# Performance work log

Hardware: AMD Instinct MI355X
Metric: run time of the kernel (lower is better)

Reference implementation:

```python
import jax, jax.numpy as jnp
import numpy as np

IMPOSSIBLE = -10000.0  # DataConfig.IMPOSSIBLE_SCORE
B, L, V, E, H, T = 64, 512, 50000, 256, 512, 32


def setup_inputs() -> dict:
    key = jax.random.key(0)
    ks = jax.random.split(key, 15)
    s = 0.05
    return {
        "sents": jax.random.randint(ks[0], (B, L), 0, V),
        "lengths": jnp.full((B,), L, dtype=jnp.int32),
        "targets": jax.random.randint(ks[1], (B, L, T), 0, 2).astype(jnp.int32),
        "emb": jax.random.normal(ks[2], (V, E), jnp.float32) * s,
        "Wih_f": jax.random.normal(ks[3], (4 * H, E), jnp.float32) * s,
        "Whh_f": jax.random.normal(ks[4], (4 * H, H), jnp.float32) * s,
        "b_f": jax.random.normal(ks[5], (4 * H,), jnp.float32) * s,
        "Wih_b": jax.random.normal(ks[6], (4 * H, E), jnp.float32) * s,
        "Whh_b": jax.random.normal(ks[7], (4 * H, H), jnp.float32) * s,
        "b_b": jax.random.normal(ks[8], (4 * H,), jnp.float32) * s,
        "W_out": jax.random.normal(ks[9], (T, 2 * H), jnp.float32) * s,
        "b_out": jax.random.normal(ks[10], (T,), jnp.float32) * s,
        "start_trans": jax.random.normal(ks[11], (T,), jnp.float32),
        "end_trans": jax.random.normal(ks[12], (T,), jnp.float32),
        "trans": jnp.ones((T, T), jnp.float32) / T,
    }


def _lstm_dir(xW, Whh, reverse):
    # xW: (L, B, 4H) = x @ Wih.T + b, precomputed (the big GEMM, done once)
    h0 = jnp.zeros((xW.shape[1], Whh.shape[1]), xW.dtype)
    def step(carry, xw):
        h, c = carry
        g = xw + h @ Whh.T
        i, f, gg, o = jnp.split(g, 4, axis=-1)  # torch gate order i,f,g,o
        c = jax.nn.sigmoid(f) * c + jax.nn.sigmoid(i) * jnp.tanh(gg)
        h = jax.nn.sigmoid(o) * jnp.tanh(c)
        return (h, c), h
    _, hs = jax.lax.scan(step, (h0, h0), xW, reverse=reverse)
    return hs  # (L, B, H), in original time order


def _denominator(em, trans, start, end):
    # em: (L, B, T); CRF partition function via forward algorithm (mask = all ones)
    alpha0 = start + em[0]
    def step(alpha, e):
        inner = alpha[:, :, None] + trans[None] + e[:, None, :]  # (B, T, T)
        return jax.nn.logsumexp(inner, axis=1), None
    alpha, _ = jax.lax.scan(step, alpha0, em[1:])
    return jax.nn.logsumexp(alpha + end[None, :], axis=-1)  # (B,)


def _numerator(em, pt, trans, start, end):
    # em: (L, B, T); pt: (L, B, T) binary possible-tag mask (float)
    alpha0 = start + em[0]
    alpha0 = jnp.where(pt[0] == 0, IMPOSSIBLE, alpha0)
    def step(alpha, inputs):
        e, cur, nxt = inputs  # each (B, T)
        e = jnp.where(nxt == 0, IMPOSSIBLE, e)
        tr = jnp.where(cur[:, :, None] == 0, IMPOSSIBLE, trans[None])
        tr = jnp.where(nxt[:, None, :] == 0, IMPOSSIBLE, tr)
        inner = alpha[:, :, None] + e[:, None, :] + tr
        return jax.nn.logsumexp(inner, axis=1), None
    alpha, _ = jax.lax.scan(step, alpha0, (em[1:], pt[:-1], pt[1:]))
    et = end[None, :] * pt[-1]
    et = jnp.where(et == 0, IMPOSSIBLE, et)
    return jax.nn.logsumexp(alpha + et, axis=-1)  # (B,)


def reference(sents, lengths, targets, emb, Wih_f, Whh_f, b_f, Wih_b, Whh_b, b_b,
              W_out, b_out, start_trans, end_trans, trans):
    x = emb[sents]                      # (B, L, E)
    x = jnp.transpose(x, (1, 0, 2))     # (L, B, E) time-major
    hf = _lstm_dir(jnp.einsum('lbe,ge->lbg', x, Wih_f) + b_f, Whh_f, False)
    hb = _lstm_dir(jnp.einsum('lbe,ge->lbg', x, Wih_b) + b_b, Whh_b, True)
    em = jnp.einsum('lbh,th->lbt', jnp.concatenate([hf, hb], axis=-1), W_out) + b_out  # (L,B,T)
    pt = jnp.transpose(targets, (1, 0, 2)).astype(em.dtype)  # (L, B, T)
    gold = _numerator(em, pt, trans, start_trans, end_trans)
    fwd = _denominator(em, trans, start_trans, end_trans)
    return jnp.sum(fwd - gold)
```

## Files before the change

### kernel.cpp

```cpp
#include <hip/hip_runtime.h>


#define IMPOSSIBLE -10000.0f

typedef __attribute__((ext_vector_type(8))) short bf16x8;
typedef __attribute__((ext_vector_type(4))) float f32x4;
typedef unsigned int u32;
typedef unsigned short u16;

__device__ __forceinline__ u16 f2b(float f) {
  union { float f; u32 u; } v; v.f = f;
  return (u16)((v.u + 0x7fffu + ((v.u >> 16) & 1u)) >> 16);
}
__device__ __forceinline__ float sigm(float x) { return 1.0f / (1.0f + __expf(-x)); }
__device__ __forceinline__ float tanh_f(float x) { return 1.0f - 2.0f / (__expf(2.0f * x) + 1.0f); }

__global__ void k_init(u32* __restrict__ flg, float* __restrict__ out) {
  const int i = blockIdx.x * 256 + threadIdx.x;
  if (i < 4096)
    __hip_atomic_store(flg + i, 0u, __ATOMIC_RELAXED, __HIP_MEMORY_SCOPE_AGENT);
  if (i == 4096)
    __hip_atomic_store((u32*)out, 0u, __ATOMIC_RELAXED, __HIP_MEMORY_SCOPE_AGENT);
}

__global__ __launch_bounds__(256) void k_embed(
    const int* __restrict__ sents, const float* __restrict__ emb,
    u16* __restrict__ x2) {
  __shared__ int tok[64];
  const int tid = threadIdx.x, t = blockIdx.x;
  if (tid < 64) tok[tid] = sents[tid * 512 + t];
  __syncthreads();
#pragma unroll
  for (int i = 0; i < 16; ++i) {
    const int v = i * 256 + tid;
    const int row = v >> 6, ke = (v & 63) * 4;
    const float4 f = *(const float4*)(emb + (size_t)tok[row] * 256 + ke);
    ushort4 s; s.x = f2b(f.x); s.y = f2b(f.y); s.z = f2b(f.z); s.w = f2b(f.w);
    *(ushort4*)&x2[((size_t)t * 64 + row) * 256 + ke] = s;
  }
}

__global__ __launch_bounds__(256, 1) void k_lstm(
    const float* __restrict__ Whf, const float* __restrict__ Whb,
    const float* __restrict__ Wif, const float* __restrict__ Wib,
    const float* __restrict__ bf_, const float* __restrict__ bb_,
    const u16* __restrict__ x2, u16* __restrict__ H2, u32* __restrict__ flg) {
  __shared__ float pre4[4096];
  const int tid = threadIdx.x, wid = blockIdx.x;
  const int r = wid & 7, d = r >> 2, g = r & 3, s = wid >> 3;
  const int b0 = g * 16, j0 = s * 16;
  const float* __restrict__ Whh = d ? Whb : Whf;
  const float* __restrict__ Wih = d ? Wib : Wif;
  const float* __restrict__ bias = d ? bb_ : bf_;
  const int wv = tid >> 6, lane = tid & 63, lm = lane & 15, kh = lane >> 4;
  const int bl = tid >> 4, jj = tid & 15;

  bf16x8 wih_f[8], whh_f[16];
#pragma unroll
  for (int gg = 0; gg < 4; ++gg) {
    const float* wp = Wih + (size_t)(gg * 512 + j0 + lm) * 256 + wv * 64;
#pragma unroll
    for (int kt = 0; kt < 2; ++kt) {
      bf16x8 f;
#pragma unroll
      for (int j = 0; j < 8; ++j) f[j] = (short)f2b(wp[kt * 32 + kh * 8 + j]);
      wih_f[gg * 2 + kt] = f;
    }
    const float* wq = Whh + (size_t)(gg * 512 + j0 + lm) * 512 + wv * 128;
#pragma unroll
    for (int kt = 0; kt < 4; ++kt) {
      bf16x8 f;
#pragma unroll
      for (int j = 0; j < 8; ++j) f[j] = (short)f2b(wq[kt * 32 + kh * 8 + j]);
      whh_f[gg * 4 + kt] = f;
    }
  }
  const float b_i = bias[0 * 512 + j0 + jj];
  const float b_f = bias[1 * 512 + j0 + jj];
  const float b_g = bias[2 * 512 + j0 + jj];
  const float b_o = bias[3 * 512 + j0 + jj];

  u32* gflg = flg + (size_t)r * 512;
  float c = 0.f;
  const f32x4 z = {0.f, 0.f, 0.f, 0.f};
#pragma unroll 1
  for (int it = 0; it < 512; ++it) {
    const int tt = d ? (511 - it) : it;
    bf16x8 xa[2];
    {
      const u16* xp = x2 + ((size_t)tt * 64 + b0 + lm) * 256 + wv * 64 + kh * 8;
      xa[0] = *(const bf16x8*)xp;
      xa[1] = *(const bf16x8*)(xp + 32);
    }
    if (it > 0) {
      if (lane < 8) {
        const u32* fp = gflg + (wv * 8 + lane) * 16;
        int bud = 1 << 16;
        while (__hip_atomic_load(fp, __ATOMIC_RELAXED, __HIP_MEMORY_SCOPE_AGENT) <
                   (u32)it && --bud) {}
      }
      asm volatile("" ::: "memory");
    }
    f32x4 accg[4] = {z, z, z, z};
#pragma unroll
    for (int gg = 0; gg < 4; ++gg)
#pragma unroll
      for (int kt = 0; kt < 2; ++kt)
        accg[gg] = __builtin_amdgcn_mfma_f32_16x16x32_bf16(xa[kt], wih_f[gg * 2 + kt], accg[gg], 0, 0, 0);
    if (it > 0) {
      const int tp = d ? (tt + 1) : (tt - 1);
      bf16x8 ha[4];
#pragma unroll
      for (int kt = 0; kt < 4; ++kt) {
        const int sG = wv * 8 + kt * 2 + (kh >> 1);
        const u16* hp = H2 + ((((size_t)tp * 2 + d) * 4 + g) * 32 + sG) * 256 + lm * 16 + (kh & 1) * 8;
        ha[kt] = *(const bf16x8*)hp;
      }
#pragma unroll
      for (int gg = 0; gg < 4; ++gg)
#pragma unroll
        for (int kt = 0; kt < 4; ++kt)
          accg[gg] = __builtin_amdgcn_mfma_f32_16x16x32_bf16(ha[kt], whh_f[gg * 4 + kt], accg[gg], 0, 0, 0);
    }
#pragma unroll
    for (int gg = 0; gg < 4; ++gg)
      *(f32x4*)&pre4[wv * 1024 + gg * 256 + kh * 64 + lm * 4] = accg[gg];
    __syncthreads();
    const int off = (bl >> 2) * 64 + jj * 4 + (bl & 3);
    float pi = b_i, pf = b_f, pg = b_g, po = b_o;
#pragma unroll
    for (int w = 0; w < 4; ++w) {
      pi += pre4[w * 1024 + 0   + off];
      pf += pre4[w * 1024 + 256 + off];
      pg += pre4[w * 1024 + 512 + off];
      po += pre4[w * 1024 + 768 + off];
    }
    c = sigm(pf) * c + sigm(pi) * tanh_f(pg);
    const float h = sigm(po) * tanh_f(c);
    const float hq = __shfl_xor(h, 1);
    if ((tid & 1) == 0) {
      const u32 pk = (u32)f2b(h) | ((u32)f2b(hq) << 16);
      u32* hp2 = (u32*)H2 + ((((size_t)tt * 2 + d) * 4 + g) * 32 + s) * 128 + (tid >> 1);
      __hip_atomic_store(hp2, pk, __ATOMIC_RELAXED, __HIP_MEMORY_SCOPE_AGENT);
    }
    asm volatile("s_waitcnt vmcnt(0)" ::: "memory");
    __syncthreads();
    if (tid == 0)
      __hip_atomic_store(gflg + s * 16, (u32)(it + 1), __ATOMIC_RELAXED,
                         __HIP_MEMORY_SCOPE_AGENT);
  }
}

__global__ __launch_bounds__(256) void k_emproj(
    const u16* __restrict__ H2, const float* __restrict__ Wo,
    const float* __restrict__ bo, float* __restrict__ em) {
  __shared__ u16 Wl[32 * 1024];
  const int tid = threadIdx.x, mb = blockIdx.x;
  const int wv = tid >> 6, lane = tid & 63, lm = lane & 15, kh = lane >> 4;
#pragma unroll
  for (int i = 0; i < 32; ++i) {
    const int row = i, k = tid * 4;
    const float4 f = *(const float4*)(Wo + (size_t)row * 1024 + k);
    ushort4 s; s.x = f2b(f.x); s.y = f2b(f.y); s.z = f2b(f.z); s.w = f2b(f.w);
    *(ushort4*)&Wl[row * 1024 + ((k + 8 * row) & 1023)] = s;
  }
  __syncthreads();
  const f32x4 z = {0.f, 0.f, 0.f, 0.f};
  f32x4 acc[2] = {z, z};
#pragma unroll 2
  for (int kt = 0; kt < 32; ++kt) {
    const int dd = kt >> 4;
    const int sG = (kt & 15) * 2 + (kh >> 1);
    const u16* ap = H2 + ((((size_t)mb * 2 + dd) * 4 + wv) * 32 + sG) * 256 + lm * 16 + (kh & 1) * 8;
    const bf16x8 a = *(const bf16x8*)ap;
#pragma unroll
    for (int ni = 0; ni < 2; ++ni) {
      const int row = ni * 16 + lm;
      const bf16x8 b = *(const bf16x8*)&Wl[row * 1024 + ((kt * 32 + kh * 8 + 8 * row) & 1023)];
      acc[ni] = __builtin_amdgcn_mfma_f32_16x16x32_bf16(a, b, acc[ni], 0, 0, 0);
    }
  }
#pragma unroll
  for (int ni = 0; ni < 2; ++ni) {
    const int n = ni * 16 + lm;
    const float bv = bo[n];
#pragma unroll
    for (int rr = 0; rr < 4; ++rr) {
      const int m = mb * 64 + wv * 16 + kh * 4 + rr;
      em[(size_t)m * 32 + n] = acc[ni][rr] + bv;
    }
  }
}

__global__ __launch_bounds__(64) void k_crf(
    const float* __restrict__ em, const int* __restrict__ tgt,
    const float* __restrict__ trans, const float* __restrict__ stt,
    const float* __restrict__ ent, float* __restrict__ out) {
  const int lane = threadIdx.x;
  const int b = blockIdx.x >> 1;
  const int isnum = blockIdx.x & 1;
  const int k = lane & 31, j0 = (lane >> 5) * 16;
  float tr[16];
#pragma unroll
  for (int j = 0; j < 16; ++j) tr[j] = trans[(j0 + j) * 32 + k];

  float an; int nxt;
  {
    float a0 = stt[k] + em[(size_t)b * 32 + k];
    int p0 = 1;
    if (isnum) { p0 = tgt[((size_t)b * 512) * 32 + k]; if (p0 == 0) a0 = IMPOSSIBLE; }
    an = a0; nxt = p0;
  }
  u32 cmask = (u32)__ballot(nxt != 0);

  const size_t eb = (size_t)b * 32 + k;
  const size_t tb = (size_t)b * 16384 + k;
  float e1 = em[eb + 1 * 2048], e2 = em[eb + 2 * 2048];
  float e3 = em[eb + 3 * 2048], e4 = em[eb + 4 * 2048];
  int g1 = 1, g2 = 1, g3 = 1, g4 = 1;
  if (isnum) {
    g1 = tgt[tb + 1 * 32]; g2 = tgt[tb + 2 * 32];
    g3 = tgt[tb + 3 * 32]; g4 = tgt[tb + 4 * 32];
  }

  auto step = [&](float e_raw, int nx) {
    const u32 cm = cmask >> j0;
    float vv[16];
#pragma unroll
    for (int j = 0; j < 16; ++j) {
      const float a = __shfl(an, j0 + j);
      float t_ = tr[j];
      if (isnum && ((((cm >> j) & 1u) == 0u) || nx == 0)) t_ = IMPOSSIBLE;
      vv[j] = a + t_;
    }
    const float m0 = fmaxf(fmaxf(fmaxf(vv[0], vv[1]), fmaxf(vv[2], vv[3])),
                           fmaxf(fmaxf(vv[4], vv[5]), fmaxf(vv[6], vv[7])));
    const float m1 = fmaxf(fmaxf(fmaxf(vv[8], vv[9]), fmaxf(vv[10], vv[11])),
                           fmaxf(fmaxf(vv[12], vv[13]), fmaxf(vv[14], vv[15])));
    const float m = fmaxf(m0, m1);
    float ss = 0.f;
#pragma unroll
    for (int j = 0; j < 16; ++j) ss += __expf(vv[j] - m);
    const float m2 = __shfl_xor(m, 32);
    const float s2 = __shfl_xor(ss, 32);
    const float M = fmaxf(m, m2);
    const float S = ss * __expf(m - M) + s2 * __expf(m2 - M);
    const float e = (isnum && nx == 0) ? IMPOSSIBLE : e_raw;
    an = M + __logf(S) + e;
    nxt = nx;
    if (isnum) cmask = (u32)__ballot(nx != 0);
  };

#pragma unroll 1
  for (int t = 1; t <= 505; t += 4) {
    const int t7 = (t + 7 < 512) ? (t + 7) : 511;
    const float n1 = em[eb + (size_t)(t + 4) * 2048];
    const float n2 = em[eb + (size_t)(t + 5) * 2048];
    const float n3 = em[eb + (size_t)(t + 6) * 2048];
    const float n4 = em[eb + (size_t)t7 * 2048];
    int h1 = 1, h2 = 1, h3 = 1, h4 = 1;
    if (isnum) {
      h1 = tgt[tb + (size_t)(t + 4) * 32]; h2 = tgt[tb + (size_t)(t + 5) * 32];
      h3 = tgt[tb + (size_t)(t + 6) * 32]; h4 = tgt[tb + (size_t)t7 * 32];
    }
    step(e1, g1); step(e2, g2); step(e3, g3); step(e4, g4);
    e1 = n1; e2 = n2; e3 = n3; e4 = n4;
    g1 = h1; g2 = h2; g3 = h3; g4 = h4;
  }
  step(e1, g1); step(e2, g2); step(e3, g3);

  float x;
  if (!isnum) {
    x = an + ent[k];
  } else {
    const float et = ent[k] * (float)nxt;
    x = an + ((et == 0.f) ? IMPOSSIBLE : et);
  }
  float m = x;
#pragma unroll
  for (int o = 1; o < 32; o <<= 1) m = fmaxf(m, __shfl_xor(m, o));
  float ss = __expf(x - m);
#pragma unroll
  for (int o = 1; o < 32; o <<= 1) ss += __shfl_xor(ss, o);
  if (lane == 0) {
    const float rr = m + __logf(ss);
    atomicAdd(out, isnum ? -rr : rr);
  }
}

extern "C" void kernel_launch(void* const* d_in, const int* in_sizes, int n_in,
                              void* d_out, int out_size, void* d_ws, size_t ws_size,
                              hipStream_t stream) {
  (void)in_sizes; (void)n_in; (void)out_size; (void)ws_size;
  const int* sents = (const int*)d_in[0];
  const int* tgt = (const int*)d_in[2];
  const float* emb = (const float*)d_in[3];
  const float* Wif = (const float*)d_in[4];
  const float* Whf = (const float*)d_in[5];
  const float* bf_ = (const float*)d_in[6];
  const float* Wib = (const float*)d_in[7];
  const float* Whb = (const float*)d_in[8];
  const float* bb_ = (const float*)d_in[9];
  const float* Wo = (const float*)d_in[10];
  const float* bo = (const float*)d_in[11];
  const float* stt = (const float*)d_in[12];
  const float* ent = (const float*)d_in[13];
  const float* trans = (const float*)d_in[14];
  float* out = (float*)d_out;

  char* ws = (char*)d_ws;
  u16* x2 = (u16*)ws;
  u16* H2 = (u16*)(ws + 16777216ull);
  float* em = (float*)(ws + 83886080ull);
  u32* flg = (u32*)(ws + 88080384ull);

  k_init<<<dim3(17), dim3(256), 0, stream>>>(flg, out);
  k_embed<<<dim3(512), dim3(256), 0, stream>>>(sents, emb, x2);
  k_lstm<<<dim3(256), dim3(256), 0, stream>>>(Whf, Whb, Wif, Wib, bf_, bb_, x2, H2, flg);
  k_emproj<<<dim3(512), dim3(256), 0, stream>>>(H2, Wo, bo, em);
  k_crf<<<dim3(128), dim3(64), 0, stream>>>(em, tgt, trans, stt, ent, out);
}
```

Baseline: 1.620 ms.

## Replace per-step flag barrier with canary-based polling on hidden-state data

Removes the per-block step flags and the store-drain/barrier/flag-store handshake in the LSTM recurrence. Instead, H2 is pre-filled with a canary value, and consumers poll the actual hidden-state words with atomic loads until no canary remains, then feed them directly to the MFMAs. This cuts one round-trip of global flag latency per timestep. In exchange, an extra kernel must fill the whole 64MB H2 buffer, and a real bf16 pair that equals the canary would stall until the poll budget runs out.

New measurement: 2.414 ms. +49.0%, slower.

```diff
diff --git a/kernel.cpp b/kernel.cpp
--- a/kernel.cpp
+++ b/kernel.cpp
@@ -2,6 +2,7 @@
 
 
 #define IMPOSSIBLE -10000.0f
+#define CANARY 0x7FFF7FFFu
 
 typedef __attribute__((ext_vector_type(8))) short bf16x8;
 typedef __attribute__((ext_vector_type(4))) float f32x4;
@@ -15,11 +16,15 @@
 __device__ __forceinline__ float sigm(float x) { return 1.0f / (1.0f + __expf(-x)); }
 __device__ __forceinline__ float tanh_f(float x) { return 1.0f - 2.0f / (__expf(2.0f * x) + 1.0f); }
 
-__global__ void k_init(u32* __restrict__ flg, float* __restrict__ out) {
-  const int i = blockIdx.x * 256 + threadIdx.x;
-  if (i < 4096)
-    __hip_atomic_store(flg + i, 0u, __ATOMIC_RELAXED, __HIP_MEMORY_SCOPE_AGENT);
-  if (i == 4096)
+__global__ __launch_bounds__(256) void k_init(u32* __restrict__ H2w,
+                                              float* __restrict__ out) {
+  const int tid = threadIdx.x;
+  const size_t b0 = (size_t)blockIdx.x * 1024;
+#pragma unroll
+  for (int k = 0; k < 4; ++k)
+    __hip_atomic_store(H2w + b0 + k * 256 + tid, CANARY, __ATOMIC_RELAXED,
+                       __HIP_MEMORY_SCOPE_AGENT);
+  if (blockIdx.x == 0 && tid == 0)
     __hip_atomic_store((u32*)out, 0u, __ATOMIC_RELAXED, __HIP_MEMORY_SCOPE_AGENT);
 }
 
@@ -44,7 +49,7 @@
     const float* __restrict__ Whf, const float* __restrict__ Whb,
     const float* __restrict__ Wif, const float* __restrict__ Wib,
     const float* __restrict__ bf_, const float* __restrict__ bb_,
-    const u16* __restrict__ x2, u16* __restrict__ H2, u32* __restrict__ flg) {
+    const u16* __restrict__ x2, u16* __restrict__ H2) {
   __shared__ float pre4[4096];
   const int tid = threadIdx.x, wid = blockIdx.x;
   const int r = wid & 7, d = r >> 2, g = r & 3, s = wid >> 3;
@@ -80,7 +85,6 @@
   const float b_g = bias[2 * 512 + j0 + jj];
   const float b_o = bias[3 * 512 + j0 + jj];
 
-  u32* gflg = flg + (size_t)r * 512;
   float c = 0.f;
   const f32x4 z = {0.f, 0.f, 0.f, 0.f};
 #pragma unroll 1
@@ -92,14 +96,29 @@
       xa[0] = *(const bf16x8*)xp;
       xa[1] = *(const bf16x8*)(xp + 32);
     }
+    u32 w[16];
     if (it > 0) {
-      if (lane < 8) {
-        const u32* fp = gflg + (wv * 8 + lane) * 16;
-        int bud = 1 << 16;
-        while (__hip_atomic_load(fp, __ATOMIC_RELAXED, __HIP_MEMORY_SCOPE_AGENT) <
-                   (u32)it && --bud) {}
+      const int tp = d ? (tt + 1) : (tt - 1);
+      const u32* hw[4];
+#pragma unroll
+      for (int kt = 0; kt < 4; ++kt) {
+        const int sG = wv * 8 + kt * 2 + (kh >> 1);
+        hw[kt] = (const u32*)(H2 + ((((size_t)tp * 2 + d) * 4 + g) * 32 + sG) * 256 + lm * 16 + (kh & 1) * 8);
       }
-      asm volatile("" ::: "memory");
+      int bud = 4096;
+      bool bad;
+      do {
+#pragma unroll
+        for (int kt = 0; kt < 4; ++kt)
+#pragma unroll
+          for (int i2 = 0; i2 < 4; ++i2)
+            w[kt * 4 + i2] = __hip_atomic_load(hw[kt] + i2, __ATOMIC_RELAXED,
+                                               __HIP_MEMORY_SCOPE_AGENT);
+        u32 anybad = 0;
+#pragma unroll
+        for (int i2 = 0; i2 < 16; ++i2) anybad |= (u32)(w[i2] == CANARY);
+        bad = __any(anybad != 0);
+      } while (bad && --bud);
     }
     f32x4 accg[4] = {z, z, z, z};
 #pragma unroll
@@ -108,20 +127,17 @@
       for (int kt = 0; kt < 2; ++kt)
         accg[gg] = __builtin_amdgcn_mfma_f32_16x16x32_bf16(xa[kt], wih_f[gg * 2 + kt], accg[gg], 0, 0, 0);
     if (it > 0) {
-      const int tp = d ? (tt + 1) : (tt - 1);
-      bf16x8 ha[4];
 #pragma unroll
       for (int kt = 0; kt < 4; ++kt) {
-        const int sG = wv * 8 + kt * 2 + (kh >> 1);
-        const u16* hp = H2 + ((((size_t)tp * 2 + d) * 4 + g) * 32 + sG) * 256 + lm * 16 + (kh & 1) * 8;
-        ha[kt] = *(const bf16x8*)hp;
+        union { u32 u[4]; bf16x8 v; } cv;
+        cv.u[0] = w[kt * 4 + 0]; cv.u[1] = w[kt * 4 + 1];
+        cv.u[2] = w[kt * 4 + 2]; cv.u[3] = w[kt * 4 + 3];
+#pragma unroll
+        for (int gg = 0; gg < 4; ++gg)
+          accg[gg] = __builtin_amdgcn_mfma_f32_16x16x32_bf16(cv.v, whh_f[gg * 4 + kt], accg[gg], 0, 0, 0);
       }
-#pragma unroll
-      for (int gg = 0; gg < 4; ++gg)
-#pragma unroll
-        for (int kt = 0; kt < 4; ++kt)
-          accg[gg] = __builtin_amdgcn_mfma_f32_16x16x32_bf16(ha[kt], whh_f[gg * 4 + kt], accg[gg], 0, 0, 0);
-    }
+    }
+    __syncthreads();
 #pragma unroll
     for (int gg = 0; gg < 4; ++gg)
       *(f32x4*)&pre4[wv * 1024 + gg * 256 + kh * 64 + lm * 4] = accg[gg];
@@ -129,11 +145,11 @@
     const int off = (bl >> 2) * 64 + jj * 4 + (bl & 3);
     float pi = b_i, pf = b_f, pg = b_g, po = b_o;
 #pragma unroll
-    for (int w = 0; w < 4; ++w) {
-      pi += pre4[w * 1024 + 0   + off];
-      pf += pre4[w * 1024 + 256 + off];
-      pg += pre4[w * 1024 + 512 + off];
-      po += pre4[w * 1024 + 768 + off];
+    for (int w4 = 0; w4 < 4; ++w4) {
+      pi += pre4[w4 * 1024 + 0   + off];
+      pf += pre4[w4 * 1024 + 256 + off];
+      pg += pre4[w4 * 1024 + 512 + off];
+      po += pre4[w4 * 1024 + 768 + off];
     }
     c = sigm(pf) * c + sigm(pi) * tanh_f(pg);
     const float h = sigm(po) * tanh_f(c);
@@ -143,11 +159,6 @@
       u32* hp2 = (u32*)H2 + ((((size_t)tt * 2 + d) * 4 + g) * 32 + s) * 128 + (tid >> 1);
       __hip_atomic_store(hp2, pk, __ATOMIC_RELAXED, __HIP_MEMORY_SCOPE_AGENT);
     }
-    asm volatile("s_waitcnt vmcnt(0)" ::: "memory");
-    __syncthreads();
-    if (tid == 0)
-      __hip_atomic_store(gflg + s * 16, (u32)(it + 1), __ATOMIC_RELAXED,
-                         __HIP_MEMORY_SCOPE_AGENT);
   }
 }
 
@@ -312,11 +323,10 @@
   u16* x2 = (u16*)ws;
   u16* H2 = (u16*)(ws + 16777216ull);
   float* em = (float*)(ws + 83886080ull);
-  u32* flg = (u32*)(ws + 88080384ull);
-
-  k_init<<<dim3(17), dim3(256), 0, stream>>>(flg, out);
+
+  k_init<<<dim3(16384), dim3(256), 0, stream>>>((u32*)H2, out);
   k_embed<<<dim3(512), dim3(256), 0, stream>>>(sents, emb, x2);
-  k_lstm<<<dim3(256), dim3(256), 0, stream>>>(Whf, Whb, Wif, Wib, bf_, bb_, x2, H2, flg);
+  k_lstm<<<dim3(256), dim3(256), 0, stream>>>(Whf, Whb, Wif, Wib, bf_, bb_, x2, H2);
   k_emproj<<<dim3(512), dim3(256), 0, stream>>>(H2, Wo, bo, em);
   k_crf<<<dim3(128), dim3(64), 0, stream>>>(em, tgt, trans, stt, ent, out);
 }
```
